# Optimization experiments

Hardware: AMD Instinct MI355X
Metric: run time of the kernel (lower is better)

Reference implementation:

```python
import jax, jax.numpy as jnp
import numpy as np

B, L, D = 2, 1024, 768
N_LAYERS, D_STATE, D_CONV, EXPAND = 4, 16, 4, 2
D_INNER = EXPAND * D
DT_RANK = (D + 15) // 16  # 48, ceil(d_model/16) as in reference Mamba
N_CLS = 10
EPS = 1e-6


def rmsnorm(x, w):
    return x * jax.lax.rsqrt(jnp.mean(x * x, axis=-1, keepdims=True) + EPS) * w


def mamba_block(x, in_w, conv_w, conv_b, xp_w, dt_w, dt_b, A_log, D_skip, out_w):
    # x: (B, L, D)
    Bsz = x.shape[0]
    xz = jnp.einsum('bld,ed->ble', x, in_w)            # (B, L, 2*d_inner)
    xi, z = jnp.split(xz, 2, axis=-1)
    # causal depthwise conv over the sequence dim
    xc = jnp.transpose(xi, (0, 2, 1))                  # (B, d_inner, L)
    xc = jax.lax.conv_general_dilated(
        xc, conv_w[:, None, :], (1,), [(D_CONV - 1, 0)],
        dimension_numbers=('NCH', 'OIH', 'NCH'), feature_group_count=D_INNER)
    xc = jnp.transpose(xc, (0, 2, 1)) + conv_b         # (B, L, d_inner)
    xc = jax.nn.silu(xc)
    # input-dependent SSM parameters
    x_dbl = jnp.einsum('bld,ed->ble', xc, xp_w)        # (B, L, dt_rank + 2*d_state)
    dt, Bs, Cs = jnp.split(x_dbl, [DT_RANK, DT_RANK + D_STATE], axis=-1)
    delta = jax.nn.softplus(jnp.einsum('blr,dr->bld', dt, dt_w) + dt_b)  # (B, L, d_inner)
    A = -jnp.exp(A_log)                                # (d_inner, d_state)
    dA = jnp.exp(delta[..., None] * A)                 # (B, L, d_inner, d_state)
    dBu = delta[..., None] * Bs[:, :, None, :] * xc[..., None]

    def step(h, inp):
        dA_t, dBu_t, C_t = inp
        h = dA_t * h + dBu_t                           # (B, d_inner, d_state)
        y = jnp.einsum('bdn,bn->bd', h, C_t)
        return h, y

    h0 = jnp.zeros((Bsz, D_INNER, D_STATE), x.dtype)
    _, ys = jax.lax.scan(step, h0, (jnp.swapaxes(dA, 0, 1),
                                    jnp.swapaxes(dBu, 0, 1),
                                    jnp.swapaxes(Cs, 0, 1)))
    y = jnp.swapaxes(ys, 0, 1) + xc * D_skip           # (B, L, d_inner)
    y = y * jax.nn.silu(z)                             # gate
    return jnp.einsum('bld,od->blo', y, out_w)


def reference(x, norm_w, in_proj_w, conv_w, conv_b, x_proj_w, dt_proj_w, dt_proj_b,
              A_log, D_skip, out_proj_w, final_norm_w,
              head1_w, head1_b, head_norm_w, head2_w, head2_b):
    for i in range(N_LAYERS):
        res = x
        x = rmsnorm(x, norm_w[i])
        x = mamba_block(x, in_proj_w[i], conv_w[i], conv_b[i], x_proj_w[i],
                        dt_proj_w[i], dt_proj_b[i], A_log[i], D_skip[i],
                        out_proj_w[i]) + res
    x = rmsnorm(x, final_norm_w)
    last = x[:, -1, :]                                 # (B, D)
    h = last @ head1_w.T + head1_b
    h = rmsnorm(h, head_norm_w)
    h = jax.nn.gelu(h, approximate=False)              # torch nn.GELU default is exact erf
    return h @ head2_w.T + head2_b                     # (B, N_CLS)


def setup_inputs() -> dict:
    key = jax.random.key(0)
    ks = jax.random.split(key, 10)
    s = 0.02
    x = jax.random.normal(ks[0], (B, L, D), jnp.float32)
    norm_w = jnp.ones((N_LAYERS, D), jnp.float32)
    in_proj_w = s * jax.random.normal(ks[1], (N_LAYERS, 2 * D_INNER, D), jnp.float32)
    conv_w = s * jax.random.normal(ks[2], (N_LAYERS, D_INNER, D_CONV), jnp.float32)
    conv_b = jnp.zeros((N_LAYERS, D_INNER), jnp.float32)
    x_proj_w = s * jax.random.normal(ks[3], (N_LAYERS, DT_RANK + 2 * D_STATE, D_INNER), jnp.float32)
    dt_proj_w = s * jax.random.normal(ks[4], (N_LAYERS, D_INNER, DT_RANK), jnp.float32)
    dt_proj_b = jnp.full((N_LAYERS, D_INNER), -4.6, jnp.float32)  # softplus(-4.6) ~ 0.01
    A_log = jnp.log(jnp.broadcast_to(
        jnp.arange(1, D_STATE + 1, dtype=jnp.float32), (N_LAYERS, D_INNER, D_STATE)) + 0.0)
    D_skip = jnp.ones((N_LAYERS, D_INNER), jnp.float32)
    out_proj_w = s * jax.random.normal(ks[5], (N_LAYERS, D, D_INNER), jnp.float32)
    final_norm_w = jnp.ones((D,), jnp.float32)
    head1_w = s * jax.random.normal(ks[6], (D, D), jnp.float32)
    head1_b = jnp.zeros((D,), jnp.float32)
    head_norm_w = jnp.ones((D,), jnp.float32)
    head2_w = s * jax.random.normal(ks[7], (N_CLS, D), jnp.float32)
    head2_b = jnp.zeros((N_CLS,), jnp.float32)
    return {"x": x, "norm_w": norm_w, "in_proj_w": in_proj_w, "conv_w": conv_w,
            "conv_b": conv_b, "x_proj_w": x_proj_w, "dt_proj_w": dt_proj_w,
            "dt_proj_b": dt_proj_b, "A_log": A_log, "D_skip": D_skip,
            "out_proj_w": out_proj_w, "final_norm_w": final_norm_w,
            "head1_w": head1_w, "head1_b": head1_b, "head_norm_w": head_norm_w,
            "head2_w": head2_w, "head2_b": head2_b}
```

## Files before the change

kernel.cpp:

```cpp
#include <hip/hip_runtime.h>
#include <hip/hip_bf16.h>
#include <math.h>

typedef __bf16 bf16;
typedef __bf16 bf16x4 __attribute__((ext_vector_type(4)));
typedef __bf16 bf16x8 __attribute__((ext_vector_type(8)));
typedef float floatx4 __attribute__((ext_vector_type(4)));

#define BB 2
#define LL 1024
#define DD 768
#define DI 1536
#define MROWS 2048
#define NXP 80
#define DTRANK 48
#define DTPAD 64
#define DSTATE 16
#define NC 16
#define CLEN 64
#define KSPLIT 16
#define OPKS 4
#define LOG2E 1.4426950408889634f
#define TROW 132
#define SYROW 68

__device__ __forceinline__ void ld16(void* lds, const void* g) {
    __builtin_amdgcn_global_load_lds(
        (const __attribute__((address_space(1))) void*)g,
        (__attribute__((address_space(3))) void*)lds, 16, 0, 0);
}

__device__ __forceinline__ void wait_vm0() {
    asm volatile("s_waitcnt vmcnt(0)" ::: "memory");
}

__device__ __forceinline__ float row16_sum(float x) {
    float t;
    t = __int_as_float(__builtin_amdgcn_update_dpp(0, __float_as_int(x), 0x111, 0xF, 0xF, true)); x += t;
    t = __int_as_float(__builtin_amdgcn_update_dpp(0, __float_as_int(x), 0x112, 0xF, 0xF, true)); x += t;
    t = __int_as_float(__builtin_amdgcn_update_dpp(0, __float_as_int(x), 0x114, 0xF, 0xF, true)); x += t;
    t = __int_as_float(__builtin_amdgcn_update_dpp(0, __float_as_int(x), 0x118, 0xF, 0xF, true)); x += t;
    return x;
}

__device__ __forceinline__ float exp2_raw(float x) {
#if __has_builtin(__builtin_amdgcn_exp2f)
    return __builtin_amdgcn_exp2f(x);
#else
    float r; asm("v_exp_f32 %0, %1" : "=v"(r) : "v"(x)); return r;
#endif
}

#define N1 (4 * 3072 * 768)
#define N2 (4 * NXP * DI)
#define N3 (4 * DI * DTPAD)
#define N4 (4 * DD * DI)
#define N5 (4 * DSTATE * DI)
__global__ __launch_bounds__(256) void cvt_all_k(const float* __restrict__ in_proj_w,
                                                 const float* __restrict__ x_proj_w,
                                                 const float* __restrict__ dt_proj_w,
                                                 const float* __restrict__ out_proj_w,
                                                 const float* __restrict__ A_log,
                                                 bf16* __restrict__ w_in,
                                                 bf16* __restrict__ w_xp,
                                                 bf16* __restrict__ w_dt,
                                                 bf16* __restrict__ w_out,
                                                 float* __restrict__ a2T) {
    int i = blockIdx.x * 256 + threadIdx.x;
    if (i < N1) { w_in[i] = (bf16)in_proj_w[i]; return; }
    i -= N1;
    if (i < N2) { w_xp[i] = (bf16)x_proj_w[i]; return; }
    i -= N2;
    if (i < N3) {
        int row = i >> 6, c = i & 63;
        w_dt[i] = (c < DTRANK) ? (bf16)dt_proj_w[row * DTRANK + c] : (bf16)0.f;
        return;
    }
    i -= N3;
    if (i < N4) { w_out[i] = (bf16)out_proj_w[i]; return; }
    i -= N4;
    if (i < N5) {
        int layer = i / (DSTATE * DI);
        int rem   = i - layer * (DSTATE * DI);
        int n     = rem / DI;
        int d     = rem - n * DI;
        a2T[i] = -__expf(A_log[(size_t)layer * DI * DSTATE + d * DSTATE + n]) * LOG2E;
    }
}

__global__ __launch_bounds__(256) void rmsnorm_k(const float* __restrict__ x,
                                                 const float* __restrict__ w,
                                                 bf16* __restrict__ out) {
    int row = blockIdx.x;
    const float* xr = x + (size_t)row * DD;
    int tid = threadIdx.x;
    float v[3]; float ss = 0.f;
    for (int j = 0; j < 3; j++) { v[j] = xr[tid + j * 256]; ss += v[j] * v[j]; }
    for (int o = 1; o < 64; o <<= 1) ss += __shfl_xor(ss, o, 64);
    __shared__ float sred[4];
    if ((tid & 63) == 0) sred[tid >> 6] = ss;
    __syncthreads();
    float scale = rsqrtf((sred[0] + sred[1] + sred[2] + sred[3]) / (float)DD + 1e-6f);
    for (int j = 0; j < 3; j++) {
        int c = tid + j * 256;
        out[(size_t)row * DD + c] = (bf16)(v[j] * scale * w[c]);
    }
}

template <int MODE>
__global__ __launch_bounds__(256) void gemm_bt(const bf16* __restrict__ A,
                                               const bf16* __restrict__ W,
                                               float* __restrict__ Cf,
                                               bf16* __restrict__ Cb,
                                               int M, int N, int K) {
    __shared__ bf16 As[128][32];
    __shared__ bf16 Ws[128][32];
    const int tid  = threadIdx.x;
    const int m0   = blockIdx.x * 128;
    const int n0   = blockIdx.y * 128;
    const int wave = tid >> 6;
    const int lane = tid & 63;
    const int wm   = (wave >> 1) * 64;
    const int wn   = (wave & 1) * 64;
    const int lrow = lane & 15;
    const int quad = lane >> 4;

    int kbeg = 0, kend = K;
    if constexpr (MODE == 5) {
        int kseg = K / gridDim.z;
        kbeg = blockIdx.z * kseg;
        kend = kbeg + kseg;
        Cf  += (size_t)blockIdx.z * M * N;
    }

    floatx4 acc[4][4];
    for (int mi = 0; mi < 4; mi++)
        for (int ni = 0; ni < 4; ni++) acc[mi][ni] = (floatx4){0.f, 0.f, 0.f, 0.f};

    const int r0  = tid >> 2;
    const int r1  = r0 + 64;
    const int seg = (tid & 3) * 8;
    char* asb0 = (char*)As + wave * 1024;
    char* asb1 = (char*)As + 4096 + wave * 1024;
    char* wsb0 = (char*)Ws + wave * 1024;
    char* wsb1 = (char*)Ws + 4096 + wave * 1024;

    for (int kb = kbeg; kb < kend; kb += 32) {
        int gk = kb + seg;
        __syncthreads();
        ld16(asb0, A + (size_t)(m0 + r0) * K + gk);
        ld16(asb1, A + (size_t)(m0 + r1) * K + gk);
        ld16(wsb0, W + (size_t)(n0 + r0) * K + gk);
        ld16(wsb1, W + (size_t)(n0 + r1) * K + gk);
        wait_vm0();
        __syncthreads();
        bf16x8 af[4], wf[4];
        for (int mi = 0; mi < 4; mi++) af[mi] = *(const bf16x8*)&As[wm + mi * 16 + lrow][quad * 8];
        for (int ni = 0; ni < 4; ni++) wf[ni] = *(const bf16x8*)&Ws[wn + ni * 16 + lrow][quad * 8];
        for (int mi = 0; mi < 4; mi++)
            for (int ni = 0; ni < 4; ni++)
                acc[mi][ni] = __builtin_amdgcn_mfma_f32_16x16x32_bf16(af[mi], wf[ni], acc[mi][ni], 0, 0, 0);
    }
    for (int mi = 0; mi < 4; mi++) {
        int rowb = m0 + wm + mi * 16 + quad * 4;
        for (int ni = 0; ni < 4; ni++) {
            int col = n0 + wn + ni * 16 + lrow;
            for (int r = 0; r < 4; r++) {
                int row = rowb + r;
                float v = acc[mi][ni][r];
                if constexpr (MODE == 1) Cb[(size_t)row * N + col] = (bf16)v;
                else                     Cf[(size_t)row * N + col] = v;
            }
        }
    }
}

__global__ __launch_bounds__(256) void op_reduce_norm_k(const float* __restrict__ part,
                                                        const float* __restrict__ resid,
                                                        const float* __restrict__ nw,
                                                        float* __restrict__ xout,
                                                        bf16* __restrict__ xnb) {
    int row = blockIdx.x;
    int tid = threadIdx.x;
    float v[3]; float ss = 0.f;
    for (int j = 0; j < 3; j++) {
        int c = tid + j * 256;
        size_t idx = (size_t)row * DD + c;
        float s = resid[idx];
        for (int ks = 0; ks < OPKS; ks++) s += part[(size_t)ks * MROWS * DD + idx];
        v[j] = s;
        xout[idx] = s;
        ss += s * s;
    }
    for (int o = 1; o < 64; o <<= 1) ss += __shfl_xor(ss, o, 64);
    __shared__ float sred[4];
    if ((tid & 63) == 0) sred[tid >> 6] = ss;
    __syncthreads();
    float scale = rsqrtf((sred[0] + sred[1] + sred[2] + sred[3]) / (float)DD + 1e-6f);
    for (int j = 0; j < 3; j++) {
        int c = tid + j * 256;
        xnb[(size_t)row * DD + c] = (bf16)(v[j] * scale * nw[c]);
    }
}

__global__ __launch_bounds__(256) void gemm_xp(const bf16* __restrict__ A,
                                               const bf16* __restrict__ W,
                                               float* __restrict__ part) {
    __shared__ bf16 As[64][40];
    __shared__ bf16 Ws[128][40];
    const int tid  = threadIdx.x;
    const int m0   = blockIdx.x * 64;
    const int ks   = blockIdx.y;
    const int k0   = ks * (DI / KSPLIT);
    const int wave = tid >> 6;
    const int lane = tid & 63;
    const int lrow = lane & 15;
    const int quad = lane >> 4;
    const int wm   = wave * 16;

    floatx4 acc[5];
    for (int ni = 0; ni < 5; ni++) acc[ni] = (floatx4){0.f, 0.f, 0.f, 0.f};

    const int ra  = tid >> 2;
    const int rw1 = ra + 64;
    const int seg = (tid & 3) * 8;

    for (int kb = 0; kb < DI / KSPLIT; kb += 32) {
        int gk = k0 + kb + seg;
        bf16x8 va = *(const bf16x8*)(A + (size_t)(m0 + ra) * DI + gk);
        bf16x8 vw0, vw1;
        if (ra < NXP) vw0 = *(const bf16x8*)(W + (size_t)ra * DI + gk);
        else          for (int j = 0; j < 8; j++) vw0[j] = (bf16)0.f;
        if (rw1 < NXP) vw1 = *(const bf16x8*)(W + (size_t)rw1 * DI + gk);
        else           for (int j = 0; j < 8; j++) vw1[j] = (bf16)0.f;
        __syncthreads();
        *(bf16x8*)&As[ra][seg]  = va;
        *(bf16x8*)&Ws[ra][seg]  = vw0;
        *(bf16x8*)&Ws[rw1][seg] = vw1;
        __syncthreads();
        bf16x8 af = *(const bf16x8*)&As[wm + lrow][quad * 8];
        for (int ni = 0; ni < 5; ni++) {
            bf16x8 wf = *(const bf16x8*)&Ws[ni * 16 + lrow][quad * 8];
            acc[ni] = __builtin_amdgcn_mfma_f32_16x16x32_bf16(af, wf, acc[ni], 0, 0, 0);
        }
    }
    float* pout = part + (size_t)ks * MROWS * NXP;
    for (int ni = 0; ni < 5; ni++) {
        int col = ni * 16 + lrow;
        for (int r = 0; r < 4; r++) {
            int row = m0 + wm + quad * 4 + r;
            pout[(size_t)row * NXP + col] = acc[ni][r];
        }
    }
}

__global__ __launch_bounds__(256) void xp_reduce_k(const float* __restrict__ part,
                                                   float* __restrict__ xdbl,
                                                   bf16* __restrict__ dtbf) {
    int idx = blockIdx.x * 256 + threadIdx.x;
    if (idx >= MROWS * NXP) return;
    float s = 0.f;
    for (int j = 0; j < KSPLIT; j++) s += part[(size_t)j * MROWS * NXP + idx];
    xdbl[idx] = s;
    int m = idx / NXP, c = idx - m * NXP;
    if (c < DTRANK)      dtbf[m * DTPAD + c] = (bf16)s;
    else if (c < DTPAD)  dtbf[m * DTPAD + c] = (bf16)0.f;
}

__global__ __launch_bounds__(256) void conv_silu_k(const bf16* __restrict__ xz,
                                                   const float* __restrict__ cw,
                                                   const float* __restrict__ cb,
                                                   bf16* __restrict__ xcb,
                                                   bf16* __restrict__ gzb) {
    int t = blockIdx.x * 256 + threadIdx.x;
    if (t >= MROWS * (DI / 4)) return;
    int m = t / (DI / 4);
    int d = (t - m * (DI / 4)) * 4;
    int l = m & (LL - 1);
    float acc[4];
    floatx4 cwv[4];
    for (int q = 0; q < 4; q++) {
        acc[q] = cb[d + q];
        cwv[q] = *(const floatx4*)&cw[(d + q) * 4];
    }
    for (int k = 0; k < 4; k++) {
        int lp = l - 3 + k;
        if (lp >= 0) {
            bf16x4 v = *(const bf16x4*)&xz[(size_t)(m - 3 + k) * (2 * DI) + d];
            for (int q = 0; q < 4; q++) acc[q] += (float)v[q] * cwv[q][k];
        }
    }
    bf16x4 xo, go;
    bf16x4 z4 = *(const bf16x4*)&xz[(size_t)m * (2 * DI) + DI + d];
    for (int q = 0; q < 4; q++) {
        float s = acc[q] / (1.f + __expf(-acc[q]));
        xo[q] = (bf16)s;
        float zv = (float)z4[q];
        go[q] = (bf16)(zv / (1.f + __expf(-zv)));
    }
    *(bf16x4*)&xcb[(size_t)m * DI + d] = xo;
    *(bf16x4*)&gzb[(size_t)m * DI + d] = go;
}

__global__ __launch_bounds__(256) void scanA_k(const bf16* __restrict__ dtb,
                                               const bf16* __restrict__ wdt,
                                               const float* __restrict__ dtbias,
                                               const bf16* __restrict__ xcb,
                                               const float* __restrict__ xdbl,
                                               const float* __restrict__ A_log,
                                               float* __restrict__ Pbuf,
                                               float* __restrict__ Sbuf,
                                               float* __restrict__ ylbuf,
                                               float* __restrict__ scbuf) {
    const int b   = blockIdx.y;
    const int d0  = blockIdx.x * 16;
    const int c0  = blockIdx.z * 2;
    const int tid = threadIdx.x;
    const int dl  = tid >> 4;
    const int n   = tid & 15;
    const int wv  = tid >> 6;
    const int lane = tid & 63;
    const int lr  = lane & 15;
    const int q   = lane >> 4;

    const float a2 = -__expf(A_log[(size_t)(d0 + dl) * DSTATE + n]) * LOG2E;
    const float bi = dtbias[d0 + lr];

    __shared__ __align__(16) bf16  sxc[CLEN][16];
    __shared__ __align__(16) float sdpT[16][TROW];
    __shared__ __align__(16) float sbcT[16][TROW];
    __shared__ __align__(16) float syT[16][SYROW];
    __shared__ __align__(16) float sST[16][SYROW];

    const bf16x8 wf0 = *(const bf16x8*)&wdt[(size_t)(d0 + lr) * DTPAD + q * 8];
    const bf16x8 wf1 = *(const bf16x8*)&wdt[(size_t)(d0 + lr) * DTPAD + 32 + q * 8];

    auto ldA = [&](int l0, bf16x8& a0, bf16x8& a1) {
        const bf16* r = &dtb[(size_t)(b * LL + l0 + 16 * wv + lr) * DTPAD + q * 8];
        a0 = *(const bf16x8*)r;
        a1 = *(const bf16x8*)(r + 32);
    };
    auto ldBC = [&](int l0, float* Bv, float* Cv) {
        #pragma unroll
        for (int k2 = 0; k2 < 4; ++k2) {
            int ii = (tid + 256 * k2) >> 4;
            const float* p = &xdbl[(size_t)(b * LL + l0 + ii) * NXP + DTRANK + n];
            Bv[k2] = p[0];
            Cv[k2] = p[DSTATE];
        }
    };
    auto dma_x = [&](int l0) {
        if (tid < 128) {
            int r2 = tid >> 1, c2 = tid & 1;
            ld16((char*)&sxc[0][0] + (tid & ~63) * 16,
                 xcb + (size_t)(b * LL + l0 + r2) * DI + d0 + c2 * 8);
        }
    };
    auto pack = [&](bf16x8 a0, bf16x8 a1, const float* Bv, const float* Cv) {
        floatx4 dacc = (floatx4){0.f, 0.f, 0.f, 0.f};
        dacc = __builtin_amdgcn_mfma_f32_16x16x32_bf16(a0, wf0, dacc, 0, 0, 0);
        dacc = __builtin_amdgcn_mfma_f32_16x16x32_bf16(a1, wf1, dacc, 0, 0, 0);
        float vv[4], xvv[4];
        #pragma unroll
        for (int r = 0; r < 4; ++r) {
            int l = 16 * wv + q * 4 + r;
            float v = dacc[r] + bi;
            v = (v > 20.f) ? v : log1pf(__expf(v));
            vv[r] = v; xvv[r] = (float)sxc[l][lr];
        }
        int L0 = 16 * wv + q * 4;
        *(float4*)&sdpT[lr][2 * L0] =
            make_float4(vv[0], vv[0] * xvv[0], vv[1], vv[1] * xvv[1]);
        *(float4*)&sdpT[lr][2 * L0 + 4] =
            make_float4(vv[2], vv[2] * xvv[2], vv[3], vv[3] * xvv[3]);
        #pragma unroll
        for (int k2 = 0; k2 < 4; ++k2) {
            int ii = (tid + 256 * k2) >> 4;
            *(float2*)&sbcT[n][2 * ii] = make_float2(Bv[k2], Cv[k2]);
        }
    };
    auto scan_loc = [&](int c) {
        float h = 0.f, sdc = 0.f;
        const float4* dpr = (const float4*)&sdpT[dl][0];
        const float4* bcr = (const float4*)&sbcT[n][0];
        float4 dA[4], bA[4], dB2[4], bB2[4];
        float y4[4], s4[4];
        #pragma unroll
        for (int t = 0; t < 4; ++t) { dA[t] = dpr[t]; bA[t] = bcr[t]; }
        #pragma unroll
        for (int g = 0; g < 8; ++g) {
            #pragma unroll
            for (int t = 0; t < 4; ++t) {
                if (g + 1 < 8) {
                    if ((g & 1) == 0) { dB2[t] = dpr[(g + 1) * 4 + t]; bB2[t] = bcr[(g + 1) * 4 + t]; }
                    else              { dA[t]  = dpr[(g + 1) * 4 + t]; bA[t]  = bcr[(g + 1) * 4 + t]; }
                }
            }
            #pragma unroll
            for (int i = 0; i < 8; ++i) {
                float4 v = ((g & 1) == 0) ? dA[i >> 1] : dB2[i >> 1];
                float4 w = ((g & 1) == 0) ? bA[i >> 1] : bB2[i >> 1];
                float dvx = (i & 1) ? v.z : v.x;
                float dpy = (i & 1) ? v.w : v.y;
                float bx  = (i & 1) ? w.z : w.x;
                float cy  = (i & 1) ? w.w : w.y;
                float e = exp2_raw(dvx * a2);
                h = __builtin_fmaf(e, h, dpy * bx);
                sdc += dvx;
                y4[i & 3] = row16_sum(h * cy);
                s4[i & 3] = sdc;
                if ((i & 3) == 3 && n == 0) {
                    *(floatx4*)&syT[dl][g * 8 + i - 3] =
                        (floatx4){y4[0], y4[1], y4[2], y4[3]};
                    *(floatx4*)&sST[dl][g * 8 + i - 3] =
                        (floatx4){s4[0], s4[1], s4[2], s4[3]};
                }
            }
        }
        size_t o = (((size_t)c * BB + b) * DI + (d0 + dl)) * DSTATE + n;
        Pbuf[o] = exp2_raw(a2 * sdc);
        Sbuf[o] = h;
    };
    auto emit = [&](int l0) {
        #pragma unroll
        for (int k2 = 0; k2 < 4; ++k2) {
            int idx = tid + 256 * k2, ii = idx >> 4, dd = idx & 15;
            size_t go = (size_t)(b * LL + l0 + ii) * DI + d0 + dd;
            ylbuf[go] = syT[dd][ii];
            scbuf[go] = sST[dd][ii];
        }
    };

    const int l0 = c0 * CLEN;
    bf16x8 a0, a1, a0n, a1n;
    float Bv[4], Cv[4], Bvn[4], Cvn[4];

    ldA(l0, a0, a1);
    ldBC(l0, Bv, Cv);
    dma_x(l0);
    wait_vm0();
    __syncthreads();

    pack(a0, a1, Bv, Cv);
    __syncthreads();
    ldA(l0 + CLEN, a0n, a1n);
    ldBC(l0 + CLEN, Bvn, Cvn);
    dma_x(l0 + CLEN);
    scan_loc(c0);
    __syncthreads();
    wait_vm0();
    emit(l0);
    __syncthreads();

    pack(a0n, a1n, Bvn, Cvn);
    __syncthreads();
    scan_loc(c0 + 1);
    __syncthreads();
    emit(l0 + CLEN);
}

__global__ __launch_bounds__(256) void compose_k(const float* __restrict__ P,
                                                 const float* __restrict__ S,
                                                 float* __restrict__ H0T) {
    int idx = blockIdx.x * 256 + threadIdx.x;
    const size_t stride = (size_t)BB * DI * DSTATE;
    int b = idx / (DI * DSTATE);
    int rest = idx - b * (DI * DSTATE);
    int d = rest >> 4;
    int n = rest & 15;
    float h = 0.f;
    #pragma unroll
    for (int c = 0; c < NC; ++c) {
        H0T[((size_t)c * BB + b) * (DSTATE * DI) + (size_t)n * DI + d] = h;
        h = __builtin_fmaf(P[(size_t)c * stride + idx], h, S[(size_t)c * stride + idx]);
    }
}

__global__ __launch_bounds__(256) void corr_k(const float* __restrict__ ylbuf,
                                              const float* __restrict__ scbuf,
                                              const float* __restrict__ xdbl,
                                              const float* __restrict__ H0T,
                                              const float* __restrict__ a2T,
                                              const bf16* __restrict__ xcb,
                                              const bf16* __restrict__ gzb,
                                              const float* __restrict__ Dskip,
                                              bf16* __restrict__ ybf) {
    const int b = blockIdx.y, c = blockIdx.z;
    const int tid = threadIdx.x;
    const int t6 = blockIdx.x * 256 + tid;
    const int dq   = (t6 % 384) * 4;
    const int loff = t6 / 384;

    __shared__ __align__(16) float sC[CLEN][16];
    {
        int l = tid >> 2, nn = (tid & 3) * 4;
        *(float4*)&sC[l][nn] =
            *(const float4*)&xdbl[(size_t)(b * LL + c * CLEN + l) * NXP + DTRANK + DSTATE + nn];
    }
    __syncthreads();

    const float* h0base = H0T + ((size_t)c * BB + b) * (DSTATE * DI);
    int m0_ = b * LL + c * CLEN + loff;
    floatx4 acc[4];
    float4 sc[4];
    #pragma unroll
    for (int s = 0; s < 4; ++s) {
        size_t mo = (size_t)(m0_ + s * 16) * DI + dq;
        sc[s] = *(const float4*)&scbuf[mo];
        float4 yl = *(const float4*)&ylbuf[mo];
        acc[s] = (floatx4){yl.x, yl.y, yl.z, yl.w};
    }
    #pragma unroll
    for (int n = 0; n < DSTATE; ++n) {
        float4 a2v = *(const float4*)&a2T[(size_t)n * DI + dq];
        float4 h0v = *(const float4*)&h0base[(size_t)n * DI + dq];
        #pragma unroll
        for (int s = 0; s < 4; ++s) {
            float Cn = sC[loff + s * 16][n];
            acc[s][0] = __builtin_fmaf(Cn * h0v.x, exp2_raw(a2v.x * sc[s].x), acc[s][0]);
            acc[s][1] = __builtin_fmaf(Cn * h0v.y, exp2_raw(a2v.y * sc[s].y), acc[s][1]);
            acc[s][2] = __builtin_fmaf(Cn * h0v.z, exp2_raw(a2v.z * sc[s].z), acc[s][2]);
            acc[s][3] = __builtin_fmaf(Cn * h0v.w, exp2_raw(a2v.w * sc[s].w), acc[s][3]);
        }
    }
    float4 Dsk = *(const float4*)&Dskip[dq];
    #pragma unroll
    for (int s = 0; s < 4; ++s) {
        size_t mo = (size_t)(m0_ + s * 16) * DI + dq;
        bf16x4 xc4 = *(const bf16x4*)&xcb[mo];
        bf16x4 gz4 = *(const bf16x4*)&gzb[mo];
        bf16x4 yo;
        yo[0] = (bf16)((acc[s][0] + (float)xc4[0] * Dsk.x) * (float)gz4[0]);
        yo[1] = (bf16)((acc[s][1] + (float)xc4[1] * Dsk.y) * (float)gz4[1]);
        yo[2] = (bf16)((acc[s][2] + (float)xc4[2] * Dsk.z) * (float)gz4[2]);
        yo[3] = (bf16)((acc[s][3] + (float)xc4[3] * Dsk.w) * (float)gz4[3]);
        *(bf16x4*)&ybf[mo] = yo;
    }
}

__global__ __launch_bounds__(256) void head_norm_k(const float* __restrict__ x,
                                                   const float* __restrict__ fnw,
                                                   float* __restrict__ xn_buf) {
    int b = blockIdx.x;
    int tid = threadIdx.x;
    const float* xr = x + ((size_t)b * LL + (LL - 1)) * DD;
    __shared__ float sred[4];
    float v[3]; float ss = 0.f;
    for (int j = 0; j < 3; j++) { v[j] = xr[tid + j * 256]; ss += v[j] * v[j]; }
    for (int o = 1; o < 64; o <<= 1) ss += __shfl_xor(ss, o, 64);
    if ((tid & 63) == 0) sred[tid >> 6] = ss;
    __syncthreads();
    float scale = rsqrtf((sred[0] + sred[1] + sred[2] + sred[3]) / (float)DD + 1e-6f);
    for (int j = 0; j < 3; j++) {
        int c = tid + j * 256;
        xn_buf[(size_t)b * DD + c] = v[j] * scale * fnw[c];
    }
}

__global__ __launch_bounds__(256) void head_h1_k(const float* __restrict__ xn_buf,
                                                 const float* __restrict__ h1w,
                                                 const float* __restrict__ h1b,
                                                 float* __restrict__ h_buf) {
    int b  = blockIdx.x;
    int o0 = blockIdx.y * 64;
    int tid = threadIdx.x;
    __shared__ float sx[DD];
    for (int c = tid; c < DD; c += 256) sx[c] = xn_buf[(size_t)b * DD + c];
    __syncthreads();
    int wave = tid >> 6, lane = tid & 63;
    for (int j = 0; j < 16; j++) {
        int o = o0 + wave * 16 + j;
        const float* wrow = h1w + (size_t)o * DD;
        float acc = 0.f;
        for (int k = 0; k < 12; k++) {
            int c = lane + 64 * k;
            acc += wrow[c] * sx[c];
        }
        for (int off = 1; off < 64; off <<= 1) acc += __shfl_xor(acc, off, 64);
        if (lane == 0) h_buf[(size_t)b * DD + o] = acc + h1b[o];
    }
}

__global__ __launch_bounds__(256) void head_out_k(const float* __restrict__ h_buf,
                                                  const float* __restrict__ hnw,
                                                  const float* __restrict__ h2w,
                                                  const float* __restrict__ h2b,
                                                  float* __restrict__ out) {
    int b = blockIdx.x;
    int tid = threadIdx.x;
    __shared__ float hh[DD];
    __shared__ float sred[4];
    const float* hr = h_buf + (size_t)b * DD;
    float ss = 0.f;
    for (int c = tid; c < DD; c += 256) { float v = hr[c]; ss += v * v; }
    for (int o = 1; o < 64; o <<= 1) ss += __shfl_xor(ss, o, 64);
    if ((tid & 63) == 0) sred[tid >> 6] = ss;
    __syncthreads();
    float sc = rsqrtf((sred[0] + sred[1] + sred[2] + sred[3]) / (float)DD + 1e-6f);
    for (int c = tid; c < DD; c += 256) {
        float v = hr[c] * sc * hnw[c];
        hh[c] = 0.5f * v * (1.f + erff(v * 0.70710678118f));
    }
    __syncthreads();
    int w = tid >> 6, lane = tid & 63;
    for (int j = w; j < 10; j += 4) {
        float acc = 0.f;
        const float* wrow = h2w + (size_t)j * DD;
        for (int c = lane; c < DD; c += 64) acc += hh[c] * wrow[c];
        for (int o = 1; o < 64; o <<= 1) acc += __shfl_xor(acc, o, 64);
        if (lane == 0) out[b * 10 + j] = acc + h2b[j];
    }
}

extern "C" void kernel_launch(void* const* d_in, const int* in_sizes, int n_in,
                              void* d_out, int out_size, void* d_ws, size_t ws_size,
                              hipStream_t stream) {
    const float* x_in      = (const float*)d_in[0];
    const float* norm_w    = (const float*)d_in[1];
    const float* in_proj_w = (const float*)d_in[2];
    const float* conv_w    = (const float*)d_in[3];
    const float* conv_b    = (const float*)d_in[4];
    const float* x_proj_w  = (const float*)d_in[5];
    const float* dt_proj_w = (const float*)d_in[6];
    const float* dt_proj_b = (const float*)d_in[7];
    const float* A_log     = (const float*)d_in[8];
    const float* D_skip    = (const float*)d_in[9];
    const float* out_proj_w= (const float*)d_in[10];
    const float* fnw       = (const float*)d_in[11];
    const float* h1w       = (const float*)d_in[12];
    const float* h1b       = (const float*)d_in[13];
    const float* hnw       = (const float*)d_in[14];
    const float* h2w       = (const float*)d_in[15];
    const float* h2b       = (const float*)d_in[16];
    float* out = (float*)d_out;

    char* ws = (char*)d_ws;
    size_t off = 0;
    auto alloc = [&](size_t bytes) -> void* {
        void* p = ws + off;
        off += (bytes + 255) & ~(size_t)255;
        return p;
    };
    bf16* w_in  = (bf16*)alloc((size_t)N1 * 2);
    bf16* w_xp  = (bf16*)alloc((size_t)N2 * 2);
    bf16* w_dt  = (bf16*)alloc((size_t)N3 * 2);
    bf16* w_out = (bf16*)alloc((size_t)N4 * 2);
    float* a2T  = (float*)alloc((size_t)N5 * 4);
    bf16* xn_bf = (bf16*)alloc((size_t)MROWS * DD * 2);
    bf16* xz_bf = (bf16*)alloc((size_t)MROWS * 2 * DI * 2);
    bf16* xc_bf = (bf16*)alloc((size_t)MROWS * DI * 2);
    bf16* gz_bf = (bf16*)alloc((size_t)MROWS * DI * 2);
    float* xdbl = (float*)alloc((size_t)MROWS * NXP * 4);
    bf16* dt_bf = (bf16*)alloc((size_t)MROWS * DTPAD * 2);
    bf16* y_bf  = (bf16*)alloc((size_t)MROWS * DI * 2);
    float* x_buf= (float*)alloc((size_t)MROWS * DD * 4);
    float* Pbuf = (float*)alloc((size_t)NC * BB * DI * DSTATE * 4);
    float* Sbuf = (float*)alloc((size_t)NC * BB * DI * DSTATE * 4);
    float* H0T  = (float*)alloc((size_t)NC * BB * DI * DSTATE * 4);
    float* ylbuf= (float*)alloc((size_t)MROWS * DI * 4);
    float* scbuf= (float*)alloc((size_t)MROWS * DI * 4);
    float* xnl  = (float*)alloc((size_t)BB * DD * 4);
    float* hbuf = (float*)alloc((size_t)BB * DD * 4);
    float* xp_part = (float*)alloc((size_t)KSPLIT * MROWS * NXP * 4);
    float* op_part = (float*)alloc((size_t)OPKS * MROWS * DD * 4);

    {
        int ntot = N1 + N2 + N3 + N4 + N5;
        cvt_all_k<<<(ntot + 255) / 256, 256, 0, stream>>>(
            in_proj_w, x_proj_w, dt_proj_w, out_proj_w, A_log,
            w_in, w_xp, w_dt, w_out, a2T);
    }

    for (int i = 0; i < 4; i++) {
        const float* x_src = (i == 0) ? x_in : x_buf;
        if (i == 0)
            rmsnorm_k<<<MROWS, 256, 0, stream>>>(x_src, norm_w, xn_bf);
        gemm_bt<1><<<dim3(MROWS / 128, 3072 / 128), 256, 0, stream>>>(
            xn_bf, w_in + (size_t)i * 3072 * 768, nullptr, xz_bf,
            MROWS, 2 * DI, DD);
        conv_silu_k<<<(MROWS * (DI / 4) + 255) / 256, 256, 0, stream>>>(
            xz_bf, conv_w + (size_t)i * DI * 4, conv_b + (size_t)i * DI, xc_bf, gz_bf);
        gemm_xp<<<dim3(MROWS / 64, KSPLIT), 256, 0, stream>>>(
            xc_bf, w_xp + (size_t)i * NXP * DI, xp_part);
        xp_reduce_k<<<(MROWS * NXP + 255) / 256, 256, 0, stream>>>(xp_part, xdbl, dt_bf);
        scanA_k<<<dim3(DI / 16, BB, NC / 2), 256, 0, stream>>>(
            dt_bf, w_dt + (size_t)i * DI * DTPAD, dt_proj_b + (size_t)i * DI,
            xc_bf, xdbl, A_log + (size_t)i * DI * DSTATE, Pbuf, Sbuf, ylbuf, scbuf);
        compose_k<<<(BB * DI * DSTATE) / 256, 256, 0, stream>>>(Pbuf, Sbuf, H0T);
        corr_k<<<dim3(24, BB, NC), 256, 0, stream>>>(
            ylbuf, scbuf, xdbl, H0T, a2T + (size_t)i * DSTATE * DI,
            xc_bf, gz_bf, D_skip + (size_t)i * DI, y_bf);
        gemm_bt<5><<<dim3(MROWS / 128, DD / 128, OPKS), 256, 0, stream>>>(
            y_bf, w_out + (size_t)i * DD * DI, op_part, nullptr,
            MROWS, DD, DI);
        op_reduce_norm_k<<<MROWS, 256, 0, stream>>>(
            op_part, x_src, norm_w + ((i + 1) & 3) * DD, x_buf, xn_bf);
    }

    head_norm_k<<<BB, 256, 0, stream>>>(x_buf, fnw, xnl);
    head_h1_k<<<dim3(BB, DD / 64), 256, 0, stream>>>(xnl, h1w, h1b, hbuf);
    head_out_k<<<BB, 256, 0, stream>>>(hbuf, hnw, h2w, h2b, out);
}
```

Baseline: 660.3 us.

## Process one chunk per scan block, interleave yl/sc output, use fast softplus

The chunked-scan kernel now handles a single 64-step chunk per block instead of two software-pipelined chunks, doubling the grid along the chunk axis. The local-scan outputs (yl and sc) are written interleaved as float2 into one buffer, and the correction kernel reads them back with paired float4 loads. Softplus now uses raw hardware exp2/log2 instead of log1pf(expf). This trades the prefetch overlap inside a block for more blocks and fewer store streams, and the fast softplus loses a little accuracy for small arguments.

```diff
diff --git a/kernel.cpp b/kernel.cpp
--- a/kernel.cpp
+++ b/kernel.cpp
@@ -21,6 +21,7 @@
 #define KSPLIT 16
 #define OPKS 4
 #define LOG2E 1.4426950408889634f
+#define LN2   0.6931471805599453f
 #define TROW 132
 #define SYROW 68
 
@@ -49,6 +50,18 @@
 #else
     float r; asm("v_exp_f32 %0, %1" : "=v"(r) : "v"(x)); return r;
 #endif
+}
+__device__ __forceinline__ float log2_raw(float x) {
+#if __has_builtin(__builtin_amdgcn_logf)
+    return __builtin_amdgcn_logf(x);
+#else
+    float r; asm("v_log_f32 %0, %1" : "=v"(r) : "v"(x)); return r;
+#endif
+}
+__device__ __forceinline__ float softplus_fast(float v) {
+    float t  = exp2_raw(v * LOG2E);
+    float sp = log2_raw(1.f + t) * LN2;
+    return (v > 20.f) ? v : sp;
 }
 
 #define N1 (4 * 3072 * 768)
@@ -310,11 +323,10 @@
                                                const float* __restrict__ A_log,
                                                float* __restrict__ Pbuf,
                                                float* __restrict__ Sbuf,
-                                               float* __restrict__ ylbuf,
-                                               float* __restrict__ scbuf) {
+                                               float2* __restrict__ ylsc) {
     const int b   = blockIdx.y;
     const int d0  = blockIdx.x * 16;
-    const int c0  = blockIdx.z * 2;
+    const int c   = blockIdx.z;
     const int tid = threadIdx.x;
     const int dl  = tid >> 4;
     const int n   = tid & 15;
@@ -322,6 +334,7 @@
     const int lane = tid & 63;
     const int lr  = lane & 15;
     const int q   = lane >> 4;
+    const int l0  = c * CLEN;
 
     const float a2 = -__expf(A_log[(size_t)(d0 + dl) * DSTATE + n]) * LOG2E;
     const float bi = dtbias[d0 + lr];
@@ -335,28 +348,29 @@
     const bf16x8 wf0 = *(const bf16x8*)&wdt[(size_t)(d0 + lr) * DTPAD + q * 8];
     const bf16x8 wf1 = *(const bf16x8*)&wdt[(size_t)(d0 + lr) * DTPAD + 32 + q * 8];
 
-    auto ldA = [&](int l0, bf16x8& a0, bf16x8& a1) {
+    bf16x8 a0, a1;
+    {
         const bf16* r = &dtb[(size_t)(b * LL + l0 + 16 * wv + lr) * DTPAD + q * 8];
         a0 = *(const bf16x8*)r;
         a1 = *(const bf16x8*)(r + 32);
-    };
-    auto ldBC = [&](int l0, float* Bv, float* Cv) {
-        #pragma unroll
-        for (int k2 = 0; k2 < 4; ++k2) {
-            int ii = (tid + 256 * k2) >> 4;
-            const float* p = &xdbl[(size_t)(b * LL + l0 + ii) * NXP + DTRANK + n];
-            Bv[k2] = p[0];
-            Cv[k2] = p[DSTATE];
-        }
-    };
-    auto dma_x = [&](int l0) {
-        if (tid < 128) {
-            int r2 = tid >> 1, c2 = tid & 1;
-            ld16((char*)&sxc[0][0] + (tid & ~63) * 16,
-                 xcb + (size_t)(b * LL + l0 + r2) * DI + d0 + c2 * 8);
-        }
-    };
-    auto pack = [&](bf16x8 a0, bf16x8 a1, const float* Bv, const float* Cv) {
+    }
+    float Bv[4], Cv[4];
+    #pragma unroll
+    for (int k2 = 0; k2 < 4; ++k2) {
+        int ii = (tid + 256 * k2) >> 4;
+        const float* p = &xdbl[(size_t)(b * LL + l0 + ii) * NXP + DTRANK + n];
+        Bv[k2] = p[0];
+        Cv[k2] = p[DSTATE];
+    }
+    if (tid < 128) {
+        int r2 = tid >> 1, c2 = tid & 1;
+        ld16((char*)&sxc[0][0] + (tid & ~63) * 16,
+             xcb + (size_t)(b * LL + l0 + r2) * DI + d0 + c2 * 8);
+    }
+    wait_vm0();
+    __syncthreads();
+
+    {
         floatx4 dacc = (floatx4){0.f, 0.f, 0.f, 0.f};
         dacc = __builtin_amdgcn_mfma_f32_16x16x32_bf16(a0, wf0, dacc, 0, 0, 0);
         dacc = __builtin_amdgcn_mfma_f32_16x16x32_bf16(a1, wf1, dacc, 0, 0, 0);
@@ -364,9 +378,8 @@
         #pragma unroll
         for (int r = 0; r < 4; ++r) {
             int l = 16 * wv + q * 4 + r;
-            float v = dacc[r] + bi;
-            v = (v > 20.f) ? v : log1pf(__expf(v));
-            vv[r] = v; xvv[r] = (float)sxc[l][lr];
+            vv[r]  = softplus_fast(dacc[r] + bi);
+            xvv[r] = (float)sxc[l][lr];
         }
         int L0 = 16 * wv + q * 4;
         *(float4*)&sdpT[lr][2 * L0] =
@@ -378,8 +391,10 @@
             int ii = (tid + 256 * k2) >> 4;
             *(float2*)&sbcT[n][2 * ii] = make_float2(Bv[k2], Cv[k2]);
         }
-    };
-    auto scan_loc = [&](int c) {
+    }
+    __syncthreads();
+
+    {
         float h = 0.f, sdc = 0.f;
         const float4* dpr = (const float4*)&sdpT[dl][0];
         const float4* bcr = (const float4*)&sbcT[n][0];
@@ -420,43 +435,15 @@
         size_t o = (((size_t)c * BB + b) * DI + (d0 + dl)) * DSTATE + n;
         Pbuf[o] = exp2_raw(a2 * sdc);
         Sbuf[o] = h;
-    };
-    auto emit = [&](int l0) {
-        #pragma unroll
-        for (int k2 = 0; k2 < 4; ++k2) {
-            int idx = tid + 256 * k2, ii = idx >> 4, dd = idx & 15;
-            size_t go = (size_t)(b * LL + l0 + ii) * DI + d0 + dd;
-            ylbuf[go] = syT[dd][ii];
-            scbuf[go] = sST[dd][ii];
-        }
-    };
-
-    const int l0 = c0 * CLEN;
-    bf16x8 a0, a1, a0n, a1n;
-    float Bv[4], Cv[4], Bvn[4], Cvn[4];
-
-    ldA(l0, a0, a1);
-    ldBC(l0, Bv, Cv);
-    dma_x(l0);
-    wait_vm0();
-    __syncthreads();
-
-    pack(a0, a1, Bv, Cv);
-    __syncthreads();
-    ldA(l0 + CLEN, a0n, a1n);
-    ldBC(l0 + CLEN, Bvn, Cvn);
-    dma_x(l0 + CLEN);
-    scan_loc(c0);
-    __syncthreads();
-    wait_vm0();
-    emit(l0);
-    __syncthreads();
-
-    pack(a0n, a1n, Bvn, Cvn);
-    __syncthreads();
-    scan_loc(c0 + 1);
-    __syncthreads();
-    emit(l0 + CLEN);
+    }
+    __syncthreads();
+
+    #pragma unroll
+    for (int k2 = 0; k2 < 4; ++k2) {
+        int idx = tid + 256 * k2, ii = idx >> 4, dd = idx & 15;
+        ylsc[(size_t)(b * LL + l0 + ii) * DI + d0 + dd] =
+            make_float2(syT[dd][ii], sST[dd][ii]);
+    }
 }
 
 __global__ __launch_bounds__(256) void compose_k(const float* __restrict__ P,
@@ -476,8 +463,7 @@
     }
 }
 
-__global__ __launch_bounds__(256) void corr_k(const float* __restrict__ ylbuf,
-                                              const float* __restrict__ scbuf,
+__global__ __launch_bounds__(256) void corr_k(const float2* __restrict__ ylsc,
                                               const float* __restrict__ xdbl,
                                               const float* __restrict__ H0T,
                                               const float* __restrict__ a2T,
@@ -506,9 +492,10 @@
     #pragma unroll
     for (int s = 0; s < 4; ++s) {
         size_t mo = (size_t)(m0_ + s * 16) * DI + dq;
-        sc[s] = *(const float4*)&scbuf[mo];
-        float4 yl = *(const float4*)&ylbuf[mo];
-        acc[s] = (floatx4){yl.x, yl.y, yl.z, yl.w};
+        float4 u0 = *(const float4*)&ylsc[mo];
+        float4 u1 = *(const float4*)&ylsc[mo + 2];
+        acc[s] = (floatx4){u0.x, u0.z, u1.x, u1.z};
+        sc[s]  = make_float4(u0.y, u0.w, u1.y, u1.w);
     }
     #pragma unroll
     for (int n = 0; n < DSTATE; ++n) {
@@ -657,8 +644,7 @@
     float* Pbuf = (float*)alloc((size_t)NC * BB * DI * DSTATE * 4);
     float* Sbuf = (float*)alloc((size_t)NC * BB * DI * DSTATE * 4);
     float* H0T  = (float*)alloc((size_t)NC * BB * DI * DSTATE * 4);
-    float* ylbuf= (float*)alloc((size_t)MROWS * DI * 4);
-    float* scbuf= (float*)alloc((size_t)MROWS * DI * 4);
+    float2* ylsc= (float2*)alloc((size_t)MROWS * DI * 8);
     float* xnl  = (float*)alloc((size_t)BB * DD * 4);
     float* hbuf = (float*)alloc((size_t)BB * DD * 4);
     float* xp_part = (float*)alloc((size_t)KSPLIT * MROWS * NXP * 4);
@@ -683,12 +669,12 @@
         gemm_xp<<<dim3(MROWS / 64, KSPLIT), 256, 0, stream>>>(
             xc_bf, w_xp + (size_t)i * NXP * DI, xp_part);
         xp_reduce_k<<<(MROWS * NXP + 255) / 256, 256, 0, stream>>>(xp_part, xdbl, dt_bf);
-        scanA_k<<<dim3(DI / 16, BB, NC / 2), 256, 0, stream>>>(
+        scanA_k<<<dim3(DI / 16, BB, NC), 256, 0, stream>>>(
             dt_bf, w_dt + (size_t)i * DI * DTPAD, dt_proj_b + (size_t)i * DI,
-            xc_bf, xdbl, A_log + (size_t)i * DI * DSTATE, Pbuf, Sbuf, ylbuf, scbuf);
+            xc_bf, xdbl, A_log + (size_t)i * DI * DSTATE, Pbuf, Sbuf, ylsc);
         compose_k<<<(BB * DI * DSTATE) / 256, 256, 0, stream>>>(Pbuf, Sbuf, H0T);
         corr_k<<<dim3(24, BB, NC), 256, 0, stream>>>(
-            ylbuf, scbuf, xdbl, H0T, a2T + (size_t)i * DSTATE * DI,
+            ylsc, xdbl, H0T, a2T + (size_t)i * DSTATE * DI,
             xc_bf, gz_bf, D_skip + (size_t)i * DI, y_bf);
         gemm_bt<5><<<dim3(MROWS / 128, DD / 128, OPKS), 256, 0, stream>>>(
             y_bf, w_out + (size_t)i * DD * DI, op_part, nullptr,
```

Measured after the change: 626.5 us. -5.1%, faster.
